# Kernel optimization log

Measured on AMD Instinct MI355X. Metric: run time of the kernel, lower is better.

## Reference

```python
import jax, jax.numpy as jnp
import numpy as np

B, N, DIM = 64, 784, 256
N1, N2, HS, WS, M, D = 1, 4, 28, 7, 8, 2  # x_windows, y_windows, H_sp, W_sp, num_heads, d
HW = HS * WS                              # 196 tokens per window
C = DIM // M                              # 32 channels per head


def setup_inputs() -> dict:
    key = jax.random.key(0)
    ks = jax.random.split(key, 5)
    x = jax.random.normal(ks[0], (B, N, DIM), dtype=jnp.float32)
    Wc = jax.random.normal(ks[1], (DIM, M * D), dtype=jnp.float32) * 0.02
    bc = jax.random.normal(ks[2], (M * D,), dtype=jnp.float32) * 0.02
    Wg = jax.random.normal(ks[3], (HW * D, HW * HW), dtype=jnp.float32) * 0.02
    bg = jax.random.normal(ks[4], (HW * HW,), dtype=jnp.float32) * 0.02
    return {"x": x, "Wc": Wc, "bc": bc, "Wg": Wg, "bg": bg}


def reference(x, Wc, bc, Wg, bg):
    b = x.shape[0]
    # compress: B N C -> B N (m d)
    w = x @ Wc + bc
    # rearrange 'b (n1 h n2 w) (m d) -> b (n1 n2 m) (h w d)'
    w = w.reshape(b, N1, HS, N2, WS, M, D)
    w = w.transpose(0, 1, 3, 5, 2, 4, 6).reshape(b, N1 * N2 * M, HW * D)
    # generate per-window mixing weights: B Nw (HW*HW)
    w = w @ Wg + bg
    w = w.reshape(b, N1 * N2 * M, HW, HW)
    # softmax over dim=-2 (the (h1 w1) source axis)
    w = jax.nn.softmax(w, axis=-2)
    # rearrange x: 'b (n1 h1 n2 w1) (m c) -> b (n1 n2 m) c (h1 w1)'
    xv = x.reshape(b, N1, HS, N2, WS, M, C)
    xv = xv.transpose(0, 1, 3, 5, 6, 2, 4).reshape(b, N1 * N2 * M, C, HW)
    # windowed mixing matmul: (b, Nw, C, HW) @ (b, Nw, HW, HW)
    out = jnp.matmul(xv, w)
    # rearrange back: 'b (n1 n2 m) c (h2 w2) -> b (n1 h2 n2 w2) (m c)'
    out = out.reshape(b, N1, N2, M, C, HS, WS)
    out = out.transpose(0, 1, 5, 2, 6, 3, 4).reshape(b, N1 * HS * N2 * WS, M * C)
    return out
```

## Files before the change

### kernel.cpp

```cpp
#include <hip/hip_runtime.h>
#include <hip/hip_bf16.h>
#include <stdint.h>
#include <stddef.h>

#define NB    64
#define NTOK  784
#define DIMC  256
#define NN2   4
#define NM    8
#define NHW   196
#define NWIN  32
#define NROWS 2048
#define NK    392
#define NKP   448
#define NBIG  38416
#define NIP   200
#define STROW 39200
#define STROW2 39232
#define NPT   39296
#define NTT   307
#define PTS   232

typedef __attribute__((ext_vector_type(4))) float f32x4;
typedef __attribute__((ext_vector_type(8))) short bf16x8;

static __device__ __forceinline__ float bf2f(unsigned short u) {
  union { unsigned int i; float f; } v; v.i = ((unsigned int)u) << 16; return v.f;
}
static __device__ __forceinline__ unsigned short f2bf(float f) {
  union { float f; unsigned int i; } v; v.f = f;
  unsigned int r = v.i + 0x7fffu + ((v.i >> 16) & 1u);
  return (unsigned short)(r >> 16);
}

__global__ __launch_bounds__(256) void k_compress(
    const float* __restrict__ x, const float* __restrict__ Wc,
    const float* __restrict__ bc, unsigned short* __restrict__ Abf) {
  __shared__ float wcs[16 * 256];
  __shared__ float bcs[16];
  const int tid = threadIdx.x;
  const int b  = blockIdx.x / NN2;
  const int n2 = blockIdx.x % NN2;
  for (int idx = tid; idx < 4096; idx += 256) {
    int c = idx >> 4, md = idx & 15;
    wcs[md * 256 + c] = Wc[idx];
  }
  if (tid < 16) bcs[tid] = bc[tid];
  __syncthreads();
  if (tid < NHW) {
    const int h = tid / 7, wcol = tid % 7;
    const int t = h * 28 + n2 * 7 + wcol;
    const float* xp = x + ((size_t)b * NTOK + t) * DIMC;
    float acc[16];
    #pragma unroll
    for (int md = 0; md < 16; ++md) acc[md] = bcs[md];
    for (int c = 0; c < 256; c += 4) {
      const f32x4 xv = *(const f32x4*)(xp + c);
      #pragma unroll
      for (int md = 0; md < 16; ++md) {
        const f32x4 wv = *(const f32x4*)(wcs + md * 256 + c);
        acc[md] += xv[0]*wv[0] + xv[1]*wv[1] + xv[2]*wv[2] + xv[3]*wv[3];
      }
    }
    #pragma unroll
    for (int md = 0; md < 16; ++md) {
      const int m = md >> 1, d = md & 1;
      const int r = b * NWIN + n2 * NM + m;
      Abf[(size_t)r * NKP + tid * 2 + d] = f2bf(acc[md]);
    }
  }
  for (int e = tid; e < NM * (NKP - NK); e += 256) {
    const int m = e / (NKP - NK);
    const int k = NK + (e % (NKP - NK));
    const int r = b * NWIN + n2 * NM + m;
    Abf[(size_t)r * NKP + k] = 0;
  }
}

__global__ __launch_bounds__(256) void k_wgt(
    const float* __restrict__ Wg, unsigned short* __restrict__ Wgbt) {
  __shared__ float tile[64][65];
  const int bid = blockIdx.x;
  const int n0 = (bid % 601) * 64;
  const int k0 = (bid / 601) * 64;
  const int tid = threadIdx.x;
  for (int idx = tid; idx < 4096; idx += 256) {
    const int kk = idx >> 6, nn = idx & 63;
    const int k = k0 + kk, n = n0 + nn;
    tile[nn][kk] = (k < NK && n < NBIG) ? Wg[(size_t)k * NBIG + n] : 0.f;
  }
  __syncthreads();
  for (int idx = tid; idx < 4096; idx += 256) {
    const int nn = idx >> 6, kk = idx & 63;
    const int n = n0 + nn;
    if (n < NBIG) {
      const int i = n / NHW, j = n % NHW;
      Wgbt[(size_t)(j * NIP + i) * NKP + (k0 + kk)] = f2bf(tile[nn][kk]);
    }
  }
}

__global__ __launch_bounds__(256) void k_zero(unsigned short* __restrict__ Wgbt) {
  const int j = blockIdx.x >> 2, i = 196 + (blockIdx.x & 3);
  unsigned int* p = (unsigned int*)(Wgbt + (size_t)(j * NIP + i) * NKP);
  if (threadIdx.x < 224) p[threadIdx.x] = 0u;
}

__global__ __launch_bounds__(256) void k_gemm(
    const unsigned short* __restrict__ A,
    const unsigned short* __restrict__ Bt,
    const float* __restrict__ bg,
    unsigned short* __restrict__ S) {
  __shared__ __align__(128) short As[128 * 64];
  __shared__ __align__(128) short Bs[128 * 64];
  const int tid = threadIdx.x;
  const int w = tid >> 6, lane = tid & 63;
  const int nwg = gridDim.x;
  const int q = nwg >> 3, rr = nwg & 7;
  const int xcd = blockIdx.x & 7, pos = blockIdx.x >> 3;
  const int wg = (xcd < rr ? xcd * (q + 1) : rr * (q + 1) + (xcd - rr) * q) + pos;
  const int mtiles = nwg / NTT;
  const int nt = wg / mtiles, mt = wg % mtiles;
  const int m0 = mt * 128, n0 = nt * 128;
  const int wm = (w >> 1) * 64, wn = (w & 1) * 64;
  const int lrow = lane >> 3, lcol = (lane & 7) * 8;
  f32x4 acc[4][4] = {};
  for (int kt = 0; kt < NKP; kt += 64) {
    #pragma unroll
    for (int is = 0; is < 4; ++is) {
      const int gg = w * 4 + is;
      const int row = gg * 8 + lrow;
      const unsigned short* ga = A  + (size_t)(m0 + row) * NKP + kt + lcol;
      const unsigned short* gb = Bt + (size_t)(n0 + row) * NKP + kt + lcol;
      __builtin_amdgcn_global_load_lds(
          (const __attribute__((address_space(1))) void*)ga,
          (__attribute__((address_space(3))) void*)((char*)As + gg * 1024), 16, 0, 0);
      __builtin_amdgcn_global_load_lds(
          (const __attribute__((address_space(1))) void*)gb,
          (__attribute__((address_space(3))) void*)((char*)Bs + gg * 1024), 16, 0, 0);
    }
    __syncthreads();
    #pragma unroll
    for (int kk = 0; kk < 2; ++kk) {
      bf16x8 af[4], bfr[4];
      #pragma unroll
      for (int i = 0; i < 4; ++i) {
        af[i]  = *(const bf16x8*)(As + (wm + i * 16 + (lane & 15)) * 64 + kk * 32 + (lane >> 4) * 8);
        bfr[i] = *(const bf16x8*)(Bs + (wn + i * 16 + (lane & 15)) * 64 + kk * 32 + (lane >> 4) * 8);
      }
      #pragma unroll
      for (int mi = 0; mi < 4; ++mi)
        #pragma unroll
        for (int ni = 0; ni < 4; ++ni)
          acc[mi][ni] = __builtin_amdgcn_mfma_f32_16x16x32_bf16(af[mi], bfr[ni], acc[mi][ni], 0, 0, 0);
    }
    __syncthreads();
  }
  #pragma unroll
  for (int ni = 0; ni < 4; ++ni) {
    const int col = n0 + wn + ni * 16 + (lane & 15);
    if (col < STROW) {
      const int i = col % NIP, j = col / NIP;
      const float bgv = (i < NHW) ? bg[i * NHW + j] : 0.f;
      #pragma unroll
      for (int mi = 0; mi < 4; ++mi)
        #pragma unroll
        for (int e = 0; e < 4; ++e) {
          const int row = m0 + wm + mi * 16 + (lane >> 4) * 4 + e;
          S[(size_t)row * STROW2 + col] = f2bf(__expf(acc[mi][ni][e] + bgv));
        }
    } else if (col < STROW2) {
      #pragma unroll
      for (int mi = 0; mi < 4; ++mi)
        #pragma unroll
        for (int e = 0; e < 4; ++e) {
          const int row = m0 + wm + mi * 16 + (lane >> 4) * 4 + e;
          S[(size_t)row * STROW2 + col] = 0;
        }
    }
  }
}

__global__ __launch_bounds__(256) void k_mix(
    const unsigned short* __restrict__ E, const float* __restrict__ x,
    float* __restrict__ out, int row0) {
  __shared__ unsigned short xvT[32 * PTS];
  const int tid = threadIdx.x, w = tid >> 6, lane = tid & 63;
  const int r = row0 + blockIdx.x;
  const int b = r >> 5, win = r & 31, n2 = win >> 3, m = win & 7;

  for (int idx = tid; idx < 1568; idx += 256) {
    const int i = idx >> 3, c4 = (idx & 7) * 4;
    const int t = (i / 7) * 28 + n2 * 7 + (i % 7);
    const f32x4 v = *(const f32x4*)(x + ((size_t)b * NTOK + t) * DIMC + m * 32 + c4);
    xvT[(c4 + 0) * PTS + i] = f2bf(v[0]);
    xvT[(c4 + 1) * PTS + i] = f2bf(v[1]);
    xvT[(c4 + 2) * PTS + i] = f2bf(v[2]);
    xvT[(c4 + 3) * PTS + i] = f2bf(v[3]);
  }
  for (int idx = tid; idx < 32 * (PTS - NHW); idx += 256) {
    const int c = idx / (PTS - NHW), i = NHW + idx % (PTS - NHW);
    xvT[c * PTS + i] = 0;
  }
  __syncthreads();

  bf16x8 bfr[2][7];
  #pragma unroll
  for (int ct = 0; ct < 2; ++ct)
    #pragma unroll
    for (int kk = 0; kk < 7; ++kk)
      bfr[ct][kk] = *(const bf16x8*)&xvT[(ct * 16 + (lane & 15)) * PTS + kk * 32 + (lane >> 4) * 8];
  const bool den = (lane & 15) == 0;
  bf16x8 oneA, oneB;
  #pragma unroll
  for (int e = 0; e < 8; ++e) {
    oneA[e] = den ? (short)0x3F80 : (short)0;
    const int i6 = 192 + (lane >> 4) * 8 + e;
    oneB[e] = (den && i6 < NHW) ? (short)0x3F80 : (short)0;
  }

  const unsigned short* Eb = E + (size_t)blockIdx.x * STROW2;
  for (int jt = w; jt < 13; jt += 4) {
    const int jA = jt * 16 + (lane & 15);
    const unsigned short* rp = Eb + (size_t)(jA < NHW ? jA : NHW - 1) * NIP + (lane >> 4) * 8;
    f32x4 a0 = {0.f,0.f,0.f,0.f}, a1 = {0.f,0.f,0.f,0.f}, ad = {0.f,0.f,0.f,0.f};
    #pragma unroll
    for (int kk = 0; kk < 7; ++kk) {
      const bf16x8 af = *(const bf16x8*)(rp + kk * 32);
      a0 = __builtin_amdgcn_mfma_f32_16x16x32_bf16(af, bfr[0][kk], a0, 0, 0, 0);
      a1 = __builtin_amdgcn_mfma_f32_16x16x32_bf16(af, bfr[1][kk], a1, 0, 0, 0);
      ad = __builtin_amdgcn_mfma_f32_16x16x32_bf16(af, (kk < 6) ? oneA : oneB, ad, 0, 0, 0);
    }
    const int c = lane & 15;
    #pragma unroll
    for (int e = 0; e < 4; ++e) {
      const int j = jt * 16 + (lane >> 4) * 4 + e;
      const float dv = __shfl(ad[e], lane & 48);
      if (j < NHW) {
        const float inv = 1.f / dv;
        const int t2 = (j / 7) * 28 + n2 * 7 + (j % 7);
        float* op = out + ((size_t)b * NTOK + t2) * DIMC + m * 32;
        op[c] = a0[e] * inv;
        op[c + 16] = a1[e] * inv;
      }
    }
  }
}

extern "C" void kernel_launch(void* const* d_in, const int* in_sizes, int n_in,
                              void* d_out, int out_size, void* d_ws, size_t ws_size,
                              hipStream_t stream) {
  const float* x  = (const float*)d_in[0];
  const float* Wc = (const float*)d_in[1];
  const float* bc = (const float*)d_in[2];
  const float* Wg = (const float*)d_in[3];
  const float* bg = (const float*)d_in[4];
  float* out = (float*)d_out;

  char* ws = (char*)d_ws;
  const size_t wgbt_bytes = (size_t)NPT * NKP * 2;
  const size_t a_bytes    = (size_t)NROWS * NKP * 2;
  unsigned short* Wgbt = (unsigned short*)ws;
  unsigned short* Abf  = (unsigned short*)(ws + wgbt_bytes);
  unsigned short* ST   = (unsigned short*)(ws + wgbt_bytes + a_bytes);
  const size_t srow_bytes = (size_t)STROW2 * 2;

  size_t avail = (ws_size > wgbt_bytes + a_bytes) ? (ws_size - wgbt_bytes - a_bytes) : 0;
  int rows_chunk = (int)(avail / srow_bytes);
  rows_chunk = (rows_chunk / 128) * 128;
  if (rows_chunk > NROWS) rows_chunk = NROWS;
  if (rows_chunk < 128)  rows_chunk = 128;

  hipLaunchKernelGGL(k_compress, dim3(NB * NN2), dim3(256), 0, stream, x, Wc, bc, Abf);
  hipLaunchKernelGGL(k_wgt, dim3(601 * 7), dim3(256), 0, stream, Wg, Wgbt);
  hipLaunchKernelGGL(k_zero, dim3(784), dim3(256), 0, stream, Wgbt);
  for (int row0 = 0; row0 < NROWS; row0 += rows_chunk) {
    int rc = NROWS - row0; if (rc > rows_chunk) rc = rows_chunk;
    hipLaunchKernelGGL(k_gemm, dim3((rc / 128) * NTT), dim3(256), 0, stream,
                       Abf + (size_t)row0 * NKP, Wgbt, bg, ST);
    hipLaunchKernelGGL(k_mix, dim3(rc), dim3(256), 0, stream, ST, x, out, row0);
  }
}
```

Baseline: 265.6 us.

## Double-buffer GEMM LDS tiles and XOR-swizzle columns to avoid bank conflicts

The main GEMM now uses two LDS buffers for A and B, so the global-to-LDS loads for the next K tile are issued before the MFMAs on the current tile run. Global column offsets are XOR-swizzled by row, and the LDS fragment reads apply the matching swizzle, to cut LDS bank conflicts. LDS use doubles to 64KB per block, which may reduce occupancy. Only one barrier per iteration remains, so correctness depends on the next stage's async writes landing in the other buffer.

```diff
diff --git a/kernel.cpp b/kernel.cpp
--- a/kernel.cpp
+++ b/kernel.cpp
@@ -111,8 +111,8 @@
     const unsigned short* __restrict__ Bt,
     const float* __restrict__ bg,
     unsigned short* __restrict__ S) {
-  __shared__ __align__(128) short As[128 * 64];
-  __shared__ __align__(128) short Bs[128 * 64];
+  __shared__ __align__(128) short As[2][128 * 64];
+  __shared__ __align__(128) short Bs[2][128 * 64];
   const int tid = threadIdx.x;
   const int w = tid >> 6, lane = tid & 63;
   const int nwg = gridDim.x;
@@ -123,30 +123,45 @@
   const int nt = wg / mtiles, mt = wg % mtiles;
   const int m0 = mt * 128, n0 = nt * 128;
   const int wm = (w >> 1) * 64, wn = (w & 1) * 64;
-  const int lrow = lane >> 3, lcol = (lane & 7) * 8;
-  f32x4 acc[4][4] = {};
-  for (int kt = 0; kt < NKP; kt += 64) {
+  const int lrow = lane >> 3;
+  const int lcolsw = ((lane & 7) ^ lrow) * 8;
+
+  const unsigned short* Arow = A  + (size_t)(m0 + w * 32 + lrow) * NKP + lcolsw;
+  const unsigned short* Brow = Bt + (size_t)(n0 + w * 32 + lrow) * NKP + lcolsw;
+
+  auto stage = [&](int kt, int buf) {
     #pragma unroll
     for (int is = 0; is < 4; ++is) {
       const int gg = w * 4 + is;
-      const int row = gg * 8 + lrow;
-      const unsigned short* ga = A  + (size_t)(m0 + row) * NKP + kt + lcol;
-      const unsigned short* gb = Bt + (size_t)(n0 + row) * NKP + kt + lcol;
       __builtin_amdgcn_global_load_lds(
-          (const __attribute__((address_space(1))) void*)ga,
-          (__attribute__((address_space(3))) void*)((char*)As + gg * 1024), 16, 0, 0);
+          (const __attribute__((address_space(1))) void*)(Arow + (size_t)is * 8 * NKP + kt),
+          (__attribute__((address_space(3))) void*)((char*)As[buf] + gg * 1024), 16, 0, 0);
       __builtin_amdgcn_global_load_lds(
-          (const __attribute__((address_space(1))) void*)gb,
-          (__attribute__((address_space(3))) void*)((char*)Bs + gg * 1024), 16, 0, 0);
-    }
-    __syncthreads();
+          (const __attribute__((address_space(1))) void*)(Brow + (size_t)is * 8 * NKP + kt),
+          (__attribute__((address_space(3))) void*)((char*)Bs[buf] + gg * 1024), 16, 0, 0);
+    }
+  };
+
+  f32x4 acc[4][4] = {};
+  stage(0, 0);
+  __syncthreads();
+  const int lq = lane >> 4;
+  const int lx = (lane & 7);
+  for (int t = 0; t < 7; ++t) {
+    const int buf = t & 1;
+    if (t < 6) stage((t + 1) * 64, buf ^ 1);
+    const short* ab = As[buf];
+    const short* bb = Bs[buf];
     #pragma unroll
     for (int kk = 0; kk < 2; ++kk) {
       bf16x8 af[4], bfr[4];
       #pragma unroll
       for (int i = 0; i < 4; ++i) {
-        af[i]  = *(const bf16x8*)(As + (wm + i * 16 + (lane & 15)) * 64 + kk * 32 + (lane >> 4) * 8);
-        bfr[i] = *(const bf16x8*)(Bs + (wn + i * 16 + (lane & 15)) * 64 + kk * 32 + (lane >> 4) * 8);
+        const int row = wm + i * 16 + (lane & 15);
+        const int slot = ((kk * 4 + lq) ^ lx) * 8;
+        af[i]  = *(const bf16x8*)(ab + row * 64 + slot);
+        const int rowb = wn + i * 16 + (lane & 15);
+        bfr[i] = *(const bf16x8*)(bb + rowb * 64 + slot);
       }
       #pragma unroll
       for (int mi = 0; mi < 4; ++mi)
@@ -156,6 +171,7 @@
     }
     __syncthreads();
   }
+
   #pragma unroll
   for (int ni = 0; ni < 4; ++ni) {
     const int col = n0 + wn + ni * 16 + (lane & 15);
```

Result: faster. 256.5 us (-3.4%).

## Pre-swizzle GEMM operands into MFMA fragment layout and fold bias into K

Applied to the files above, without the earlier changes.

Both GEMM operands are pre-permuted into MFMA fragment order (Af, Bf) so the big GEMM loads register fragments straight from global memory with double buffering, with no LDS staging or barriers. The bias is folded in as an extra K column (a ones column in A and a bg row in B). The exp output is written directly in the fragment layout that k_mix consumes, and the tile grows to 256x128 per workgroup. This trades LDS reuse for direct global fragment loads and more registers per thread. It adds an extra zeroing kernel and scattered 2-byte writes in the epilogue.

```diff
diff --git a/kernel.cpp b/kernel.cpp
--- a/kernel.cpp
+++ b/kernel.cpp
@@ -13,13 +13,13 @@
 #define NROWS 2048
 #define NK    392
 #define NKP   448
+#define KKF   13
 #define NBIG  38416
-#define NIP   200
-#define STROW 39200
-#define STROW2 39232
 #define NPT   39296
+#define NFB   2456
 #define NTT   307
 #define PTS   232
+#define WFRAG 46592
 
 typedef __attribute__((ext_vector_type(4))) float f32x4;
 typedef __attribute__((ext_vector_type(8))) short bf16x8;
@@ -73,12 +73,23 @@
     const int m = e / (NKP - NK);
     const int k = NK + (e % (NKP - NK));
     const int r = b * NWIN + n2 * NM + m;
-    Abf[(size_t)r * NKP + k] = 0;
+    Abf[(size_t)r * NKP + k] = (k == NK) ? (unsigned short)0x3F80 : 0;
+  }
+}
+
+__global__ __launch_bounds__(256) void k_afrag(
+    const unsigned short* __restrict__ A, unsigned short* __restrict__ Af) {
+  const int mf = blockIdx.x;
+  for (int idx = threadIdx.x; idx < KKF * 64; idx += 256) {
+    const int kk = idx >> 6, l = idx & 63;
+    const bf16x8 v = *(const bf16x8*)(A + (size_t)(mf * 16 + (l & 15)) * NKP + kk * 32 + (l >> 4) * 8);
+    *(bf16x8*)(Af + ((size_t)(mf * KKF + kk) * 64 + l) * 8) = v;
   }
 }
 
 __global__ __launch_bounds__(256) void k_wgt(
-    const float* __restrict__ Wg, unsigned short* __restrict__ Wgbt) {
+    const float* __restrict__ Wg, const float* __restrict__ bg,
+    unsigned short* __restrict__ Bf) {
   __shared__ float tile[64][65];
   const int bid = blockIdx.x;
   const int n0 = (bid % 601) * 64;
@@ -87,95 +98,108 @@
   for (int idx = tid; idx < 4096; idx += 256) {
     const int kk = idx >> 6, nn = idx & 63;
     const int k = k0 + kk, n = n0 + nn;
-    tile[nn][kk] = (k < NK && n < NBIG) ? Wg[(size_t)k * NBIG + n] : 0.f;
+    float v = 0.f;
+    if (n < NBIG) {
+      if (k < NK) v = Wg[(size_t)k * NBIG + n];
+      else if (k == NK) v = bg[n];
+    }
+    tile[nn][kk] = v;
   }
   __syncthreads();
-  for (int idx = tid; idx < 4096; idx += 256) {
-    const int nn = idx >> 6, kk = idx & 63;
+  for (int idx = tid; idx < 512; idx += 256) {
+    const int nn = idx >> 3, g = idx & 7;
     const int n = n0 + nn;
-    if (n < NBIG) {
+    const int kg = k0 + g * 8;
+    const int kk = kg >> 5;
+    if (n < NBIG && kk < KKF) {
       const int i = n / NHW, j = n % NHW;
-      Wgbt[(size_t)(j * NIP + i) * NKP + (k0 + kk)] = f2bf(tile[nn][kk]);
-    }
-  }
-}
-
-__global__ __launch_bounds__(256) void k_zero(unsigned short* __restrict__ Wgbt) {
-  const int j = blockIdx.x >> 2, i = 196 + (blockIdx.x & 3);
-  unsigned int* p = (unsigned int*)(Wgbt + (size_t)(j * NIP + i) * NKP);
-  if (threadIdx.x < 224) p[threadIdx.x] = 0u;
-}
-
-__global__ __launch_bounds__(256) void k_gemm(
-    const unsigned short* __restrict__ A,
-    const unsigned short* __restrict__ Bt,
-    const float* __restrict__ bg,
-    unsigned short* __restrict__ S) {
-  __shared__ __align__(128) short As[128 * 64];
-  __shared__ __align__(128) short Bs[128 * 64];
+      const int np = j * 200 + i;
+      const int lane2 = (np & 15) + ((kg >> 3) & 3) * 16;
+      bf16x8 v;
+      #pragma unroll
+      for (int e = 0; e < 8; ++e) v[e] = (short)f2bf(tile[nn][g * 8 + e]);
+      *(bf16x8*)(Bf + ((size_t)((np >> 4) * KKF + kk) * 64 + lane2) * 8) = v;
+    }
+  }
+}
+
+__global__ void k_zero(unsigned short* __restrict__ Bf) {
+  const int bid = blockIdx.x;
+  int np;
+  if (bid < 784) { const int j = bid >> 2, i = 196 + (bid & 3); np = j * 200 + i; }
+  else           { np = 39200 + (bid - 784); }
+  const int t = threadIdx.x;
+  if (t < KKF * 4) {
+    const int kk = t >> 2, q2 = t & 3;
+    bf16x8 z = {};
+    *(bf16x8*)(Bf + ((size_t)((np >> 4) * KKF + kk) * 64 + (np & 15) + q2 * 16) * 8) = z;
+  }
+}
+
+__global__ __launch_bounds__(256) void k_ezero(unsigned short* __restrict__ E) {
+  unsigned short* Ew = E + (size_t)blockIdx.x * WFRAG;
+  for (int idx = threadIdx.x; idx < 13 * 48; idx += 256) {
+    const int jf = idx / 48, l = 16 + idx % 48;
+    bf16x8 z = {};
+    *(bf16x8*)(Ew + ((size_t)(jf * 7 + 6) * 64 + l) * 8) = z;
+  }
+}
+
+__global__ __launch_bounds__(256, 2) void k_gemm(
+    const unsigned short* __restrict__ Af,
+    const unsigned short* __restrict__ Bf,
+    unsigned short* __restrict__ E, int row0, int mtiles) {
   const int tid = threadIdx.x;
   const int w = tid >> 6, lane = tid & 63;
   const int nwg = gridDim.x;
   const int q = nwg >> 3, rr = nwg & 7;
   const int xcd = blockIdx.x & 7, pos = blockIdx.x >> 3;
   const int wg = (xcd < rr ? xcd * (q + 1) : rr * (q + 1) + (xcd - rr) * q) + pos;
-  const int mtiles = nwg / NTT;
   const int nt = wg / mtiles, mt = wg % mtiles;
-  const int m0 = mt * 128, n0 = nt * 128;
-  const int wm = (w >> 1) * 64, wn = (w & 1) * 64;
-  const int lrow = lane >> 3, lcol = (lane & 7) * 8;
-  f32x4 acc[4][4] = {};
-  for (int kt = 0; kt < NKP; kt += 64) {
-    #pragma unroll
-    for (int is = 0; is < 4; ++is) {
-      const int gg = w * 4 + is;
-      const int row = gg * 8 + lrow;
-      const unsigned short* ga = A  + (size_t)(m0 + row) * NKP + kt + lcol;
-      const unsigned short* gb = Bt + (size_t)(n0 + row) * NKP + kt + lcol;
-      __builtin_amdgcn_global_load_lds(
-          (const __attribute__((address_space(1))) void*)ga,
-          (__attribute__((address_space(3))) void*)((char*)As + gg * 1024), 16, 0, 0);
-      __builtin_amdgcn_global_load_lds(
-          (const __attribute__((address_space(1))) void*)gb,
-          (__attribute__((address_space(3))) void*)((char*)Bs + gg * 1024), 16, 0, 0);
-    }
-    __syncthreads();
-    #pragma unroll
-    for (int kk = 0; kk < 2; ++kk) {
-      bf16x8 af[4], bfr[4];
-      #pragma unroll
-      for (int i = 0; i < 4; ++i) {
-        af[i]  = *(const bf16x8*)(As + (wm + i * 16 + (lane & 15)) * 64 + kk * 32 + (lane >> 4) * 8);
-        bfr[i] = *(const bf16x8*)(Bs + (wn + i * 16 + (lane & 15)) * 64 + kk * 32 + (lane >> 4) * 8);
-      }
-      #pragma unroll
-      for (int mi = 0; mi < 4; ++mi)
-        #pragma unroll
-        for (int ni = 0; ni < 4; ++ni)
-          acc[mi][ni] = __builtin_amdgcn_mfma_f32_16x16x32_bf16(af[mi], bfr[ni], acc[mi][ni], 0, 0, 0);
-    }
-    __syncthreads();
-  }
-  #pragma unroll
-  for (int ni = 0; ni < 4; ++ni) {
-    const int col = n0 + wn + ni * 16 + (lane & 15);
-    if (col < STROW) {
-      const int i = col % NIP, j = col / NIP;
-      const float bgv = (i < NHW) ? bg[i * NHW + j] : 0.f;
-      #pragma unroll
-      for (int mi = 0; mi < 4; ++mi)
+  const int wr = w >> 1, wn = w & 1;
+  const int mf0 = ((row0 + mt * 256) >> 4) + wr * 8;
+  const int nf0 = ((nt * 128) >> 4) + wn * 4;
+  const unsigned short* Ab = Af + (size_t)mf0 * KKF * 512 + lane * 8;
+  const unsigned short* Bb = Bf + (size_t)nf0 * KKF * 512 + lane * 8;
+
+  f32x4 acc[8][4] = {};
+  bf16x8 a[2][8], b[2][4];
+  #pragma unroll
+  for (int fi = 0; fi < 8; ++fi) a[0][fi] = *(const bf16x8*)(Ab + (size_t)fi * KKF * 512);
+  #pragma unroll
+  for (int fj = 0; fj < 4; ++fj) b[0][fj] = *(const bf16x8*)(Bb + (size_t)fj * KKF * 512);
+  #pragma unroll
+  for (int s = 0; s < KKF; ++s) {
+    const int cur = s & 1, nxt = cur ^ 1;
+    if (s < KKF - 1) {
+      #pragma unroll
+      for (int fi = 0; fi < 8; ++fi)
+        a[nxt][fi] = *(const bf16x8*)(Ab + ((size_t)fi * KKF + s + 1) * 512);
+      #pragma unroll
+      for (int fj = 0; fj < 4; ++fj)
+        b[nxt][fj] = *(const bf16x8*)(Bb + ((size_t)fj * KKF + s + 1) * 512);
+    }
+    #pragma unroll
+    for (int fi = 0; fi < 8; ++fi)
+      #pragma unroll
+      for (int fj = 0; fj < 4; ++fj)
+        acc[fi][fj] = __builtin_amdgcn_mfma_f32_16x16x32_bf16(a[cur][fi], b[cur][fj], acc[fi][fj], 0, 0, 0);
+  }
+
+  const int rbl = mt * 256 + wr * 128;
+  const int cq = lane >> 4, cr = lane & 15;
+  #pragma unroll
+  for (int fj = 0; fj < 4; ++fj) {
+    const int col = nt * 128 + wn * 64 + fj * 16 + cr;
+    if (col < 39200) {
+      const int j = col / 200, i = col - j * 200;
+      const size_t coff = ((size_t)((j >> 4) * 7 + (i >> 5)) * 64 + (j & 15) + ((i >> 3) & 3) * 16) * 8 + (i & 7);
+      #pragma unroll
+      for (int fi = 0; fi < 8; ++fi)
         #pragma unroll
         for (int e = 0; e < 4; ++e) {
-          const int row = m0 + wm + mi * 16 + (lane >> 4) * 4 + e;
-          S[(size_t)row * STROW2 + col] = f2bf(__expf(acc[mi][ni][e] + bgv));
-        }
-    } else if (col < STROW2) {
-      #pragma unroll
-      for (int mi = 0; mi < 4; ++mi)
-        #pragma unroll
-        for (int e = 0; e < 4; ++e) {
-          const int row = m0 + wm + mi * 16 + (lane >> 4) * 4 + e;
-          S[(size_t)row * STROW2 + col] = 0;
+          const int wl = rbl + fi * 16 + cq * 4 + e;
+          E[(size_t)wl * WFRAG + coff] = f2bf(__expf(acc[fi][fj][e]));
         }
     }
   }
@@ -219,14 +243,12 @@
     oneB[e] = (den && i6 < NHW) ? (short)0x3F80 : (short)0;
   }
 
-  const unsigned short* Eb = E + (size_t)blockIdx.x * STROW2;
+  const unsigned short* Ew = E + (size_t)blockIdx.x * WFRAG;
   for (int jt = w; jt < 13; jt += 4) {
-    const int jA = jt * 16 + (lane & 15);
-    const unsigned short* rp = Eb + (size_t)(jA < NHW ? jA : NHW - 1) * NIP + (lane >> 4) * 8;
     f32x4 a0 = {0.f,0.f,0.f,0.f}, a1 = {0.f,0.f,0.f,0.f}, ad = {0.f,0.f,0.f,0.f};
     #pragma unroll
     for (int kk = 0; kk < 7; ++kk) {
-      const bf16x8 af = *(const bf16x8*)(rp + kk * 32);
+      const bf16x8 af = *(const bf16x8*)(Ew + ((size_t)(jt * 7 + kk) * 64 + lane) * 8);
       a0 = __builtin_amdgcn_mfma_f32_16x16x32_bf16(af, bfr[0][kk], a0, 0, 0, 0);
       a1 = __builtin_amdgcn_mfma_f32_16x16x32_bf16(af, bfr[1][kk], a1, 0, 0, 0);
       ad = __builtin_amdgcn_mfma_f32_16x16x32_bf16(af, (kk < 6) ? oneA : oneB, ad, 0, 0, 0);
@@ -258,26 +280,31 @@
   float* out = (float*)d_out;
 
   char* ws = (char*)d_ws;
-  const size_t wgbt_bytes = (size_t)NPT * NKP * 2;
-  const size_t a_bytes    = (size_t)NROWS * NKP * 2;
-  unsigned short* Wgbt = (unsigned short*)ws;
-  unsigned short* Abf  = (unsigned short*)(ws + wgbt_bytes);
-  unsigned short* ST   = (unsigned short*)(ws + wgbt_bytes + a_bytes);
-  const size_t srow_bytes = (size_t)STROW2 * 2;
-
-  size_t avail = (ws_size > wgbt_bytes + a_bytes) ? (ws_size - wgbt_bytes - a_bytes) : 0;
-  int rows_chunk = (int)(avail / srow_bytes);
-  rows_chunk = (rows_chunk / 128) * 128;
+  const size_t bf_bytes = (size_t)NFB * KKF * 512 * 2;
+  const size_t a_bytes  = (size_t)NROWS * NKP * 2;
+  const size_t af_bytes = (size_t)128 * KKF * 512 * 2;
+  unsigned short* Bf  = (unsigned short*)ws;
+  unsigned short* Abf = (unsigned short*)(ws + bf_bytes);
+  unsigned short* Af  = (unsigned short*)(ws + bf_bytes + a_bytes);
+  unsigned short* E   = (unsigned short*)(ws + bf_bytes + a_bytes + af_bytes);
+  const size_t fixed = bf_bytes + a_bytes + af_bytes;
+  const size_t wrow_bytes = (size_t)WFRAG * 2;
+
+  size_t avail = (ws_size > fixed) ? (ws_size - fixed) : 0;
+  int rows_chunk = (int)(avail / wrow_bytes);
+  rows_chunk = (rows_chunk / 256) * 256;
   if (rows_chunk > NROWS) rows_chunk = NROWS;
-  if (rows_chunk < 128)  rows_chunk = 128;
+  if (rows_chunk < 256)  rows_chunk = 256;
 
   hipLaunchKernelGGL(k_compress, dim3(NB * NN2), dim3(256), 0, stream, x, Wc, bc, Abf);
-  hipLaunchKernelGGL(k_wgt, dim3(601 * 7), dim3(256), 0, stream, Wg, Wgbt);
-  hipLaunchKernelGGL(k_zero, dim3(784), dim3(256), 0, stream, Wgbt);
+  hipLaunchKernelGGL(k_afrag, dim3(128), dim3(256), 0, stream, Abf, Af);
+  hipLaunchKernelGGL(k_wgt, dim3(601 * 7), dim3(256), 0, stream, Wg, bg, Bf);
+  hipLaunchKernelGGL(k_zero, dim3(880), dim3(64), 0, stream, Bf);
   for (int row0 = 0; row0 < NROWS; row0 += rows_chunk) {
     int rc = NROWS - row0; if (rc > rows_chunk) rc = rows_chunk;
-    hipLaunchKernelGGL(k_gemm, dim3((rc / 128) * NTT), dim3(256), 0, stream,
-                       Abf + (size_t)row0 * NKP, Wgbt, bg, ST);
-    hipLaunchKernelGGL(k_mix, dim3(rc), dim3(256), 0, stream, ST, x, out, row0);
-  }
-}
+    hipLaunchKernelGGL(k_ezero, dim3(rc), dim3(256), 0, stream, E);
+    hipLaunchKernelGGL(k_gemm, dim3((rc / 256) * NTT), dim3(256), 0, stream,
+                       Af, Bf, E, row0, rc / 256);
+    hipLaunchKernelGGL(k_mix, dim3(rc), dim3(256), 0, stream, E, x, out, row0);
+  }
+}
```

Measured after the change: 371.0 us. 39.7% more time.
